# Optimization experiments

Hardware: AMD Instinct MI355X
Metric: run time of the kernel (lower is better)

## Reference

```python
import jax, jax.numpy as jnp
import numpy as np

XY, ZS, NTOK = 16, 8, 10000
N = XY * XY * ZS  # 2048 states
NEG_INF = -jnp.inf

_OFFS = np.array([[0, 0, 0], [1, 0, 0], [-1, 0, 0], [0, 1, 0], [0, -1, 0], [0, 0, 1], [0, 0, 2]], dtype=np.int32)


def transition_log_p(trans_params):
    # Vectorized version of the per-state Python loop in the torch code.
    idx = jnp.arange(N)
    z, rem = idx // (XY * XY), idx % (XY * XY)
    y, x = rem // XY, rem % XY
    offs = jnp.asarray(_OFFS)
    nx = x[:, None] + offs[None, :, 0]  # [N,7]
    ny = y[:, None] + offs[None, :, 1]
    nz = z[:, None] + offs[None, :, 2]
    valid = (nx >= 0) & (nx < XY) & (ny >= 0) & (ny < XY) & (nz >= 0) & (nz < ZS)
    # torch code softmaxes the FIRST k params of row h, where k = number of valid
    # neighbors, assigning them to valid neighbors in offset order.
    param_idx = jnp.cumsum(valid.astype(jnp.int32), axis=1) - 1  # [N,7]
    gathered = jnp.take_along_axis(trans_params, jnp.clip(param_idx, 0, 6), axis=1)
    logits = jnp.where(valid, gathered, NEG_INF)
    logp = jax.nn.log_softmax(logits, axis=1)  # invalid slots stay -inf
    nbr = (jnp.clip(nx, 0, XY - 1)
           + XY * (jnp.clip(ny, 0, XY - 1) + XY * jnp.clip(nz, 0, ZS - 1)))  # [N,7]
    nbr = jnp.where(valid, nbr, idx[:, None])  # route invalid to self slot
    vals = jnp.where(valid, logp, NEG_INF)
    rows = jnp.broadcast_to(idx[:, None], (N, 7))
    out = jnp.full((N, N), NEG_INF, dtype=trans_params.dtype)
    # scatter-max: -inf placeholders never overwrite real entries
    return out.at[rows, nbr].max(vals)


def emission_log_p_all(emis_params, stories):
    # stories: [B,T,L] int tokens. Returns [T,B,N].
    logE = jax.nn.log_softmax(emis_params, axis=1)           # [N,V]
    logE = jnp.concatenate([logE, jnp.zeros((N, 1), logE.dtype)], axis=1)  # pad col (token==-1 -> 0)
    e = jnp.take(logE, stories, axis=1)                      # [N,B,T,L]
    return e.sum(-1).transpose(2, 1, 0)                      # [T,B,N]


def setup_inputs() -> dict:
    key = jax.random.key(0)
    k1, k2, k3, k4 = jax.random.split(key, 4)
    B, T, L = 16, 16, 16
    stories = jax.random.randint(k1, (B, T, L), 0, NTOK)
    return {
        "stories_tensor": stories,
        "story_length": T,
        "trans_params": jax.random.normal(k2, (N, 7), jnp.float32),
        "emis_params": jax.random.normal(k3, (N, NTOK), jnp.float32),
        "prior_params": jax.random.normal(k4, (N,), jnp.float32),
    }


def reference(stories_tensor, story_length, trans_params, emis_params, prior_params):
    assert stories_tensor.shape[1] == story_length
    prior = jax.nn.log_softmax(prior_params, axis=0)         # [N]
    trans = transition_log_p(trans_params)                   # [N,N], mostly -inf
    emis = emission_log_p_all(emis_params, stories_tensor)   # [T,B,N]
    alpha0 = emis[0] + prior                                 # [B,N]

    def step(alpha, emis_t):
        # intermediate[b,h,j] = trans[h,j] + alpha[b,j]; logsumexp over j
        new = emis_t + jax.nn.logsumexp(trans[None, :, :] + alpha[:, None, :], axis=-1)
        return new, new

    _, rest = jax.lax.scan(step, alpha0, emis[1:])
    return jnp.concatenate([alpha0[None], rest], axis=0)     # [T,B,N]
```

## Files before the change

### kernel.cpp

```cpp
#include <hip/hip_runtime.h>
#include <math.h>

#define XY   16
#define ZS   8
#define NST  2048
#define NTOK 10000
#define BB   16
#define TT   16
#define LL   16
#define NV4  2500
#define NP   256

__global__ __launch_bounds__(256) void emis_kernel(
    const float* __restrict__ E, const int* __restrict__ stories,
    float* __restrict__ ws) {
  __shared__ __align__(16) float row[NTOK];
  __shared__ float red[4];
  const int h   = blockIdx.x;
  const int tid = threadIdx.x;
  const int lane = tid & 63, wid = tid >> 6;

  int4 st[4];
  {
    const int4* sp = reinterpret_cast<const int4*>(stories) + tid * 4;
    #pragma unroll
    for (int k = 0; k < 4; ++k) st[k] = sp[k];
  }

  const float4* E4 = reinterpret_cast<const float4*>(E + (size_t)h * NTOK);
  float4 v[10];
  #pragma unroll
  for (int k = 0; k < 10; ++k) {
    const int i = tid + k * 256;
    v[k] = E4[i < NV4 ? i : (NV4 - 1)];
  }

  float4* row4 = reinterpret_cast<float4*>(row);
  float s0 = 0.f, s1 = 0.f, s2 = 0.f, s3 = 0.f;
  #pragma unroll
  for (int k = 0; k < 10; ++k) {
    const int i  = tid + k * 256;
    const int is = i < NV4 ? i : (NV4 - 1);
    row4[is] = v[k];
    if (i < NV4) {
      s0 += __expf(v[k].x); s1 += __expf(v[k].y);
      s2 += __expf(v[k].z); s3 += __expf(v[k].w);
    }
  }
  float s = (s0 + s1) + (s2 + s3);
  #pragma unroll
  for (int off = 32; off; off >>= 1) s += __shfl_xor(s, off);
  if (lane == 0) red[wid] = s;
  __syncthreads();
  const float d = __logf(red[0] + red[1] + red[2] + red[3]);

  float sum = 0.f;
  int   cnt = 0;
  #pragma unroll
  for (int k = 0; k < 4; ++k) {
    const int t0 = st[k].x, t1 = st[k].y, t2 = st[k].z, t3 = st[k].w;
    if (t0 >= 0) { sum += row[t0]; cnt++; }
    if (t1 >= 0) { sum += row[t1]; cnt++; }
    if (t2 >= 0) { sum += row[t2]; cnt++; }
    if (t3 >= 0) { sum += row[t3]; cnt++; }
  }
  ws[(size_t)h * NP + tid] = sum - (float)cnt * d;
}

__device__ __forceinline__ float4 load_emis(const float* __restrict__ ws,
                                            int h0, int bt) {
  float4 e;
  e.x = ws[(size_t)(h0 + 0) * NP + bt];
  e.y = ws[(size_t)(h0 + 1) * NP + bt];
  e.z = ws[(size_t)(h0 + 2) * NP + bt];
  e.w = ws[(size_t)(h0 + 3) * NP + bt];
  return e;
}

#define AOFF 16
#define ASZ  (AOFF + NST + 528)

__global__ __launch_bounds__(512) void fwd_kernel(
    const float* __restrict__ trans, const float* __restrict__ prior,
    const float* __restrict__ ws, float* __restrict__ out) {
  __shared__ float s_alpha[2][ASZ];
  __shared__ float red_m[8], red_s[8];
  const int tid = threadIdx.x;
  const int b   = blockIdx.x;
  const int h0  = tid * 4;

  for (int i = tid; i < AOFF; i += 512) { s_alpha[0][i] = 0.f; s_alpha[1][i] = 0.f; }
  for (int i = AOFF + NST + tid; i < ASZ; i += 512) { s_alpha[0][i] = 0.f; s_alpha[1][i] = 0.f; }

  const float4 pr = *reinterpret_cast<const float4*>(prior + h0);
  float m = fmaxf(fmaxf(pr.x, pr.y), fmaxf(pr.z, pr.w));
  float s = __expf(pr.x - m) + __expf(pr.y - m) + __expf(pr.z - m) + __expf(pr.w - m);
  #pragma unroll
  for (int off = 32; off > 0; off >>= 1) {
    float mo = __shfl_down(m, off), so = __shfl_down(s, off);
    float mn = fmaxf(m, mo);
    s = s * __expf(m - mn) + so * __expf(mo - mn);
    m = mn;
  }
  const int lane = tid & 63, wid = tid >> 6;
  if (lane == 0) { red_m[wid] = m; red_s[wid] = s; }
  __syncthreads();
  float LZ;
  {
    float mm = red_m[0], ss = red_s[0];
    #pragma unroll
    for (int w = 1; w < 8; ++w) {
      float mo = red_m[w], so = red_s[w];
      float mn = fmaxf(mm, mo);
      ss = ss * __expf(mm - mn) + so * __expf(mo - mn);
      mm = mn;
    }
    LZ = mm + __logf(ss);
  }

  float lp[4][7];
  #pragma unroll
  for (int i = 0; i < 4; ++i) {
    const int h = h0 + i;
    const int x = h & 15, y = (h >> 4) & 15, z = h >> 8;
    bool vd[7];
    vd[0] = true;
    vd[1] = (x < XY - 1);
    vd[2] = (x > 0);
    vd[3] = (y < XY - 1);
    vd[4] = (y > 0);
    vd[5] = (z < ZS - 1);
    vd[6] = (z < ZS - 2);
    float p0 = trans[h * 7 + 0], p1 = trans[h * 7 + 1], p2 = trans[h * 7 + 2],
          p3 = trans[h * 7 + 3], p4 = trans[h * 7 + 4], p5 = trans[h * 7 + 5],
          p6 = trans[h * 7 + 6];
    float lg[7];
    #pragma unroll
    for (int o = 0; o < 7; ++o) {
      lg[o] = vd[o] ? p0 : -INFINITY;
      if (vd[o]) { p0 = p1; p1 = p2; p2 = p3; p3 = p4; p4 = p5; p5 = p6; }
    }
    float mx = lg[0];
    #pragma unroll
    for (int o = 1; o < 7; ++o) mx = fmaxf(mx, lg[o]);
    float ssum = 0.f;
    #pragma unroll
    for (int o = 0; o < 7; ++o) ssum += __expf(lg[o] - mx);
    const float lz = mx + __logf(ssum);
    #pragma unroll
    for (int o = 0; o < 7; ++o) lp[i][o] = lg[o] - lz;
  }

  {
    const float4 e0 = load_emis(ws, h0, b * 16 + 0);
    float4 a;
    a.x = e0.x + pr.x - LZ;
    a.y = e0.y + pr.y - LZ;
    a.z = e0.z + pr.z - LZ;
    a.w = e0.w + pr.w - LZ;
    *reinterpret_cast<float4*>(&s_alpha[0][AOFF + h0]) = a;
    *reinterpret_cast<float4*>(out + (size_t)b * NST + h0) = a;
  }
  __syncthreads();

  float4 e_nxt = load_emis(ws, h0, b * 16 + 1);
  int cur = 0;
  for (int t = 1; t < TT; ++t) {
    const float4 ecur = e_nxt;
    if (t + 1 < TT) e_nxt = load_emis(ws, h0, b * 16 + t + 1);

    const float* al = s_alpha[cur];
    const float4 A  = *reinterpret_cast<const float4*>(al + AOFF + h0);
    const float4 Bp = *reinterpret_cast<const float4*>(al + AOFF + h0 + 16);
    const float4 Bm = *reinterpret_cast<const float4*>(al + AOFF + h0 - 16);
    const float4 C  = *reinterpret_cast<const float4*>(al + AOFF + h0 + 256);
    const float4 D  = *reinterpret_cast<const float4*>(al + AOFF + h0 + 512);
    const float xm  = al[AOFF + h0 - 1];
    const float xp  = al[AOFF + h0 + 4];

#define STEP_STATE(i, SELF, XP, XM, YP, YM, Z1, Z2, EV, OUTV)                        \
    {                                                                                \
      float v0 = lp[i][0] + (SELF);                                                  \
      float v1 = lp[i][1] + (XP);                                                    \
      float v2 = lp[i][2] + (XM);                                                    \
      float v3 = lp[i][3] + (YP);                                                    \
      float v4 = lp[i][4] + (YM);                                                    \
      float v5 = lp[i][5] + (Z1);                                                    \
      float v6 = lp[i][6] + (Z2);                                                    \
      float mx = fmaxf(fmaxf(fmaxf(v0, v1), fmaxf(v2, v3)),                          \
                       fmaxf(fmaxf(v4, v5), v6));                                    \
      float ss = __expf(v0 - mx) + __expf(v1 - mx) + __expf(v2 - mx) +               \
                 __expf(v3 - mx) + __expf(v4 - mx) + __expf(v5 - mx) +               \
                 __expf(v6 - mx);                                                    \
      (OUTV) = (EV) + mx + __logf(ss);                                               \
    }

    float4 na;
    STEP_STATE(0, A.x, A.y, xm,  Bp.x, Bm.x, C.x, D.x, ecur.x, na.x);
    STEP_STATE(1, A.y, A.z, A.x, Bp.y, Bm.y, C.y, D.y, ecur.y, na.y);
    STEP_STATE(2, A.z, A.w, A.y, Bp.z, Bm.z, C.z, D.z, ecur.z, na.z);
    STEP_STATE(3, A.w, xp,  A.z, Bp.w, Bm.w, C.w, D.w, ecur.w, na.w);
#undef STEP_STATE

    *reinterpret_cast<float4*>(&s_alpha[cur ^ 1][AOFF + h0]) = na;
    *reinterpret_cast<float4*>(out + (size_t)(t * BB + b) * NST + h0) = na;
    __syncthreads();
    cur ^= 1;
  }
}

extern "C" void kernel_launch(void* const* d_in, const int* in_sizes, int n_in,
                              void* d_out, int out_size, void* d_ws, size_t ws_size,
                              hipStream_t stream) {
  const int*   stories = (const int*)  d_in[0];
  const float* trans   = (const float*)d_in[2];
  const float* emis    = (const float*)d_in[3];
  const float* prior   = (const float*)d_in[4];
  float* out = (float*)d_out;
  float* dws = (float*)d_ws;

  hipLaunchKernelGGL(emis_kernel, dim3(NST), dim3(256), 0, stream,
                     emis, stories, dws);
  hipLaunchKernelGGL(fwd_kernel, dim3(BB), dim3(512), 0, stream,
                     trans, prior, dws, out);
}
```

Before: 44.25 us.

## Widen emission kernel to 512 threads and preload all emissions in forward kernel

The emission kernel now uses 512 threads per state row. Each thread loads fewer float4s, and pairs of threads split the 16 tokens of a (b,t) sequence and combine their sums with a shuffle. The forward kernel preloads every timestep's emission values into registers with float4 loads at the start and fully unrolls the time loop. This replaces the per-step scalar strided global loads on the serial critical path. In exchange it raises register pressure (64 extra floats per thread) in the forward kernel.

Result: no change. 43.82 us (-1.0%).

```diff
diff --git a/kernel.cpp b/kernel.cpp
--- a/kernel.cpp
+++ b/kernel.cpp
@@ -11,35 +11,28 @@
 #define NV4  2500
 #define NP   256
 
-__global__ __launch_bounds__(256) void emis_kernel(
+__global__ __launch_bounds__(512, 8) void emis_kernel(
     const float* __restrict__ E, const int* __restrict__ stories,
     float* __restrict__ ws) {
   __shared__ __align__(16) float row[NTOK];
-  __shared__ float red[4];
+  __shared__ float red[8];
   const int h   = blockIdx.x;
   const int tid = threadIdx.x;
   const int lane = tid & 63, wid = tid >> 6;
 
-  int4 st[4];
-  {
-    const int4* sp = reinterpret_cast<const int4*>(stories) + tid * 4;
-    #pragma unroll
-    for (int k = 0; k < 4; ++k) st[k] = sp[k];
-  }
-
   const float4* E4 = reinterpret_cast<const float4*>(E + (size_t)h * NTOK);
-  float4 v[10];
-  #pragma unroll
-  for (int k = 0; k < 10; ++k) {
-    const int i = tid + k * 256;
+  float4 v[5];
+  #pragma unroll
+  for (int k = 0; k < 5; ++k) {
+    const int i = tid + k * 512;
     v[k] = E4[i < NV4 ? i : (NV4 - 1)];
   }
 
   float4* row4 = reinterpret_cast<float4*>(row);
   float s0 = 0.f, s1 = 0.f, s2 = 0.f, s3 = 0.f;
   #pragma unroll
-  for (int k = 0; k < 10; ++k) {
-    const int i  = tid + k * 256;
+  for (int k = 0; k < 5; ++k) {
+    const int i  = tid + k * 512;
     const int is = i < NV4 ? i : (NV4 - 1);
     row4[is] = v[k];
     if (i < NV4) {
@@ -52,29 +45,27 @@
   for (int off = 32; off; off >>= 1) s += __shfl_xor(s, off);
   if (lane == 0) red[wid] = s;
   __syncthreads();
-  const float d = __logf(red[0] + red[1] + red[2] + red[3]);
-
+  const float d = __logf(red[0] + red[1] + red[2] + red[3] +
+                         red[4] + red[5] + red[6] + red[7]);
+
+  const int half = tid & 1, p = tid >> 1;
+  const int4* sp = reinterpret_cast<const int4*>(stories) + p * 4 + half * 2;
+  const int4 sa = sp[0], sb = sp[1];
   float sum = 0.f;
   int   cnt = 0;
-  #pragma unroll
-  for (int k = 0; k < 4; ++k) {
-    const int t0 = st[k].x, t1 = st[k].y, t2 = st[k].z, t3 = st[k].w;
-    if (t0 >= 0) { sum += row[t0]; cnt++; }
-    if (t1 >= 0) { sum += row[t1]; cnt++; }
-    if (t2 >= 0) { sum += row[t2]; cnt++; }
-    if (t3 >= 0) { sum += row[t3]; cnt++; }
-  }
-  ws[(size_t)h * NP + tid] = sum - (float)cnt * d;
-}
-
-__device__ __forceinline__ float4 load_emis(const float* __restrict__ ws,
-                                            int h0, int bt) {
-  float4 e;
-  e.x = ws[(size_t)(h0 + 0) * NP + bt];
-  e.y = ws[(size_t)(h0 + 1) * NP + bt];
-  e.z = ws[(size_t)(h0 + 2) * NP + bt];
-  e.w = ws[(size_t)(h0 + 3) * NP + bt];
-  return e;
+  {
+    if (sa.x >= 0) { sum += row[sa.x]; cnt++; }
+    if (sa.y >= 0) { sum += row[sa.y]; cnt++; }
+    if (sa.z >= 0) { sum += row[sa.z]; cnt++; }
+    if (sa.w >= 0) { sum += row[sa.w]; cnt++; }
+    if (sb.x >= 0) { sum += row[sb.x]; cnt++; }
+    if (sb.y >= 0) { sum += row[sb.y]; cnt++; }
+    if (sb.z >= 0) { sum += row[sb.z]; cnt++; }
+    if (sb.w >= 0) { sum += row[sb.w]; cnt++; }
+  }
+  sum += __shfl_xor(sum, 1);
+  cnt += __shfl_xor(cnt, 1);
+  if (!half) ws[(size_t)h * NP + p] = sum - (float)cnt * d;
 }
 
 #define AOFF 16
@@ -88,6 +79,18 @@
   const int tid = threadIdx.x;
   const int b   = blockIdx.x;
   const int h0  = tid * 4;
+
+  float ee[4][16];
+  #pragma unroll
+  for (int i = 0; i < 4; ++i) {
+    #pragma unroll
+    for (int j = 0; j < 4; ++j) {
+      const float4 q = *reinterpret_cast<const float4*>(
+          ws + (size_t)(h0 + i) * NP + b * 16 + 4 * j);
+      ee[i][4 * j + 0] = q.x; ee[i][4 * j + 1] = q.y;
+      ee[i][4 * j + 2] = q.z; ee[i][4 * j + 3] = q.w;
+    }
+  }
 
   for (int i = tid; i < AOFF; i += 512) { s_alpha[0][i] = 0.f; s_alpha[1][i] = 0.f; }
   for (int i = AOFF + NST + tid; i < ASZ; i += 512) { s_alpha[0][i] = 0.f; s_alpha[1][i] = 0.f; }
@@ -152,23 +155,19 @@
   }
 
   {
-    const float4 e0 = load_emis(ws, h0, b * 16 + 0);
     float4 a;
-    a.x = e0.x + pr.x - LZ;
-    a.y = e0.y + pr.y - LZ;
-    a.z = e0.z + pr.z - LZ;
-    a.w = e0.w + pr.w - LZ;
+    a.x = ee[0][0] + pr.x - LZ;
+    a.y = ee[1][0] + pr.y - LZ;
+    a.z = ee[2][0] + pr.z - LZ;
+    a.w = ee[3][0] + pr.w - LZ;
     *reinterpret_cast<float4*>(&s_alpha[0][AOFF + h0]) = a;
     *reinterpret_cast<float4*>(out + (size_t)b * NST + h0) = a;
   }
   __syncthreads();
 
-  float4 e_nxt = load_emis(ws, h0, b * 16 + 1);
   int cur = 0;
+  #pragma unroll
   for (int t = 1; t < TT; ++t) {
-    const float4 ecur = e_nxt;
-    if (t + 1 < TT) e_nxt = load_emis(ws, h0, b * 16 + t + 1);
-
     const float* al = s_alpha[cur];
     const float4 A  = *reinterpret_cast<const float4*>(al + AOFF + h0);
     const float4 Bp = *reinterpret_cast<const float4*>(al + AOFF + h0 + 16);
@@ -196,10 +195,10 @@
     }
 
     float4 na;
-    STEP_STATE(0, A.x, A.y, xm,  Bp.x, Bm.x, C.x, D.x, ecur.x, na.x);
-    STEP_STATE(1, A.y, A.z, A.x, Bp.y, Bm.y, C.y, D.y, ecur.y, na.y);
-    STEP_STATE(2, A.z, A.w, A.y, Bp.z, Bm.z, C.z, D.z, ecur.z, na.z);
-    STEP_STATE(3, A.w, xp,  A.z, Bp.w, Bm.w, C.w, D.w, ecur.w, na.w);
+    STEP_STATE(0, A.x, A.y, xm,  Bp.x, Bm.x, C.x, D.x, ee[0][t], na.x);
+    STEP_STATE(1, A.y, A.z, A.x, Bp.y, Bm.y, C.y, D.y, ee[1][t], na.y);
+    STEP_STATE(2, A.z, A.w, A.y, Bp.z, Bm.z, C.z, D.z, ee[2][t], na.z);
+    STEP_STATE(3, A.w, xp,  A.z, Bp.w, Bm.w, C.w, D.w, ee[3][t], na.w);
 #undef STEP_STATE
 
     *reinterpret_cast<float4*>(&s_alpha[cur ^ 1][AOFF + h0]) = na;
@@ -219,7 +218,7 @@
   float* out = (float*)d_out;
   float* dws = (float*)d_ws;
 
-  hipLaunchKernelGGL(emis_kernel, dim3(NST), dim3(256), 0, stream,
+  hipLaunchKernelGGL(emis_kernel, dim3(NST), dim3(512), 0, stream,
                      emis, stories, dws);
   hipLaunchKernelGGL(fwd_kernel, dim3(BB), dim3(512), 0, stream,
                      trans, prior, dws, out);
```
